# Kernel tuning notes

Measured on AMD Instinct MI355X. Metric: run time of the kernel, lower is better.

Reference implementation:

```python
import jax, jax.numpy as jnp
import numpy as np

B, T, C, H = 4, 2048, 1024, 16
HS = C // H  # head_size = 64
FF = 4 * C   # 4096
EPS = 1e-5


def _layernorm(x, g, b):
    mu = jnp.mean(x, axis=-1, keepdims=True)
    var = jnp.mean(jnp.square(x - mu), axis=-1, keepdims=True)
    return (x - mu) * jax.lax.rsqrt(var + EPS) * g + b


def setup_inputs() -> dict:
    key = jax.random.key(0)
    ks = jax.random.split(key, 12)
    s_in = 1.0 / np.sqrt(C)
    s_ff = 1.0 / np.sqrt(FF)
    return {
        "x": jax.random.normal(ks[0], (B, T, C), jnp.float32),
        # per-head projection weights stacked: [H, C, HS]
        "Wq": jax.random.normal(ks[1], (H, C, HS), jnp.float32) * s_in,
        "Wk": jax.random.normal(ks[2], (H, C, HS), jnp.float32) * s_in,
        "Wv": jax.random.normal(ks[3], (H, C, HS), jnp.float32) * s_in,
        "Wo": jax.random.normal(ks[4], (C, C), jnp.float32) * s_in,
        "bo": jnp.zeros((C,), jnp.float32),
        "g1": jnp.ones((C,), jnp.float32),
        "b1": jnp.zeros((C,), jnp.float32),
        "g2": jnp.ones((C,), jnp.float32),
        "b2": jnp.zeros((C,), jnp.float32),
        "W1": jax.random.normal(ks[5], (C, FF), jnp.float32) * s_in,
        "bf1": jnp.zeros((FF,), jnp.float32),
        "W2": jax.random.normal(ks[6], (FF, C), jnp.float32) * s_ff,
        "bf2": jnp.zeros((C,), jnp.float32),
    }


def reference(x, Wq, Wk, Wv, Wo, bo, g1, b1, g2, b2, W1, bf1, W2, bf2):
    # pre-norm
    h = _layernorm(x, g1, b1)                       # [B,T,C]
    q = jnp.einsum('btc,hcd->bhtd', h, Wq)          # [B,H,T,HS]
    k = jnp.einsum('btc,hcd->bhtd', h, Wk)
    v = jnp.einsum('btc,hcd->bhtd', h, Wv)
    w = jnp.einsum('bhtd,bhsd->bhts', q, k) * (HS ** -0.5)  # [B,H,T,S]
    mask = jnp.tril(jnp.ones((T, T), bool))          # causal tril
    w = jnp.where(mask[None, None], w, -jnp.inf)
    # NB: original code softmaxes over dim=1 of [B,T,T], i.e. the QUERY axis
    w = jax.nn.softmax(w, axis=-2)
    o = jnp.einsum('bhts,bhsd->bhtd', w, v)          # [B,H,T,HS]
    o = jnp.transpose(o, (0, 2, 1, 3)).reshape(B, T, C)  # concat heads
    x = x + o @ Wo + bo                              # residual 1 (dropout=0)
    f = _layernorm(x, g2, b2)
    ff = jax.nn.relu(f @ W1 + bf1) @ W2 + bf2        # FFN (dropout=0)
    return x + ff
```

## Files before the change

### kernel.cpp

```cpp
#include <hip/hip_runtime.h>


#define T_SEQ 2048
#define SCALE2 0.1803368801f

typedef __attribute__((ext_vector_type(8))) short short8;
typedef __attribute__((ext_vector_type(4))) float f32x4;

typedef __attribute__((address_space(1))) unsigned int g_u32;
typedef __attribute__((address_space(3))) unsigned int l_u32;

__device__ __forceinline__ unsigned short f2bf(float f) {
  union { float f; unsigned u; } x; x.f = f;
  unsigned r = (x.u + 0x7FFFu + ((x.u >> 16) & 1u)) >> 16;
  return (unsigned short)r;
}
__device__ __forceinline__ float bf2f(unsigned short u) {
  union { unsigned u; float f; } x; x.u = (unsigned)u << 16;
  return x.f;
}

__device__ __forceinline__ void g2lds16(const void* g, void* l) {
  __builtin_amdgcn_global_load_lds((g_u32*)g, (l_u32*)l, 16, 0, 0);
}

__device__ __forceinline__ int xcd_swz(int flat, int nwg) {
  if ((nwg & 7) != 0) return flat;
  return (flat & 7) * (nwg >> 3) + (flat >> 3);
}

template <int EPI>
__global__ __launch_bounds__(512, 2) void gemm256(
    const unsigned short* __restrict__ A, const unsigned short* __restrict__ Bt,
    int M, int N, int K,
    unsigned short* __restrict__ out16, const float* __restrict__ bias) {
  extern __shared__ unsigned short lds[];
  unsigned short* ldsA = lds;
  unsigned short* ldsB = lds + 2 * 16384;
  const int tid = threadIdx.x, lane = tid & 63, wid = tid >> 6;
  const int wm = wid >> 2, wn = wid & 3;
  const int nx = gridDim.x;
  const int flat = blockIdx.y * nx + blockIdx.x;
  const int swz = xcd_swz(flat, nx * gridDim.y);
  const int mBase = (swz / nx) * 256, nBase = (swz % nx) * 256;

  f32x4 acc[8][4];
#pragma unroll
  for (int i = 0; i < 8; ++i)
#pragma unroll
    for (int j = 0; j < 4; ++j)
#pragma unroll
      for (int e = 0; e < 4; ++e) acc[i][j][e] = 0.f;

  auto stage = [&](int buf, int kt) {
    const int k0 = kt << 6;
#pragma unroll
    for (int it = 0; it < 4; ++it) {
      int g = it * 512 + tid;
      int row = g >> 3, colL = g & 7;
      int col = colL ^ (row & 7);
      g2lds16(A + ((size_t)(mBase + row) * K + k0 + col * 8),
              &ldsA[buf * 16384 + (it * 512 + wid * 64) * 8]);
      g2lds16(Bt + ((size_t)(nBase + row) * K + k0 + col * 8),
              &ldsB[buf * 16384 + (it * 512 + wid * 64) * 8]);
    }
  };

  const int nKT = K >> 6;
  stage(0, 0);
  __syncthreads();
  int cur = 0;
  for (int kt = 0; kt < nKT; ++kt) {
    if (kt + 1 < nKT) stage(cur ^ 1, kt + 1);

    short8 bf[4][2];
#pragma unroll
    for (int fn = 0; fn < 4; ++fn)
#pragma unroll
      for (int ks = 0; ks < 2; ++ks) {
        int r = wn * 64 + fn * 16 + (lane & 15);
        int c = (ks * 4 + (lane >> 4)) ^ (r & 7);
        bf[fn][ks] = *(const short8*)&ldsB[cur * 16384 + r * 64 + c * 8];
      }
#pragma unroll
    for (int q = 0; q < 4; ++q) {
      short8 af[2][2];
#pragma unroll
      for (int mf = 0; mf < 2; ++mf)
#pragma unroll
        for (int ks = 0; ks < 2; ++ks) {
          int r = wm * 128 + q * 32 + mf * 16 + (lane & 15);
          int c = (ks * 4 + (lane >> 4)) ^ (r & 7);
          af[mf][ks] = *(const short8*)&ldsA[cur * 16384 + r * 64 + c * 8];
        }
      __builtin_amdgcn_s_setprio(1);
#pragma unroll
      for (int mf = 0; mf < 2; ++mf)
#pragma unroll
        for (int fn = 0; fn < 4; ++fn)
#pragma unroll
          for (int ks = 0; ks < 2; ++ks)
            acc[q * 2 + mf][fn] = __builtin_amdgcn_mfma_f32_16x16x32_bf16(
                af[mf][ks], bf[fn][ks], acc[q * 2 + mf][fn], 0, 0, 0);
      __builtin_amdgcn_s_setprio(0);
    }
    __syncthreads();
    cur ^= 1;
  }

#pragma unroll
  for (int am = 0; am < 8; ++am)
#pragma unroll
    for (int fn = 0; fn < 4; ++fn) {
      int col = nBase + wn * 64 + fn * 16 + (lane & 15);
      int row0 = mBase + wm * 128 + am * 16 + ((lane >> 4) << 2);
      if (EPI == 0) {
#pragma unroll
        for (int r = 0; r < 4; ++r)
          out16[(size_t)(row0 + r) * N + col] = f2bf(acc[am][fn][r]);
      } else {
        float bv = bias[col];
#pragma unroll
        for (int r = 0; r < 4; ++r)
          out16[(size_t)(row0 + r) * N + col] =
              f2bf(fmaxf(acc[am][fn][r] + bv, 0.f));
      }
    }
}

template <int EPI>
__global__ __launch_bounds__(256) void gemm_bt(
    const unsigned short* __restrict__ A, const unsigned short* __restrict__ Bt,
    int M, int N, int K,
    unsigned short* __restrict__ out16, float* __restrict__ outF,
    const float* __restrict__ bias, const float* __restrict__ resid) {
  __shared__ unsigned short ldsA[128 * 64];
  __shared__ unsigned short ldsB[128 * 64];
  const int tid = threadIdx.x;
  const int lane = tid & 63, wid = tid >> 6;
  const int wm = wid >> 1, wn = wid & 1;
  const int nx = gridDim.x;
  const int flat = blockIdx.y * nx + blockIdx.x;
  const int swz = xcd_swz(flat, nx * gridDim.y);
  const int mBase = (swz / nx) * 128, nBase = (swz % nx) * 128;

  f32x4 acc[4][4];
#pragma unroll
  for (int i = 0; i < 4; ++i)
#pragma unroll
    for (int j = 0; j < 4; ++j)
#pragma unroll
      for (int e = 0; e < 4; ++e) acc[i][j][e] = 0.f;

  const int nKT = K >> 6;
  for (int kt = 0; kt < nKT; ++kt) {
    const int k0 = kt << 6;
#pragma unroll
    for (int it = 0; it < 4; ++it) {
      int g = it * 256 + wid * 64 + lane;
      int row = g >> 3, colL = g & 7;
      int col = colL ^ (row & 7);
      g2lds16(A + ((size_t)(mBase + row) * K + k0 + col * 8),
              &ldsA[(it * 256 + wid * 64) * 8]);
      g2lds16(Bt + ((size_t)(nBase + row) * K + k0 + col * 8),
              &ldsB[(it * 256 + wid * 64) * 8]);
    }
    __syncthreads();

    short8 af[4][2], bf[4][2];
#pragma unroll
    for (int fm = 0; fm < 4; ++fm)
#pragma unroll
      for (int ks = 0; ks < 2; ++ks) {
        int r = wm * 64 + fm * 16 + (lane & 15);
        int c = (ks * 4 + (lane >> 4)) ^ (r & 7);
        af[fm][ks] = *(const short8*)&ldsA[r * 64 + c * 8];
      }
#pragma unroll
    for (int fn = 0; fn < 4; ++fn)
#pragma unroll
      for (int ks = 0; ks < 2; ++ks) {
        int r = wn * 64 + fn * 16 + (lane & 15);
        int c = (ks * 4 + (lane >> 4)) ^ (r & 7);
        bf[fn][ks] = *(const short8*)&ldsB[r * 64 + c * 8];
      }
    __builtin_amdgcn_s_setprio(1);
#pragma unroll
    for (int fm = 0; fm < 4; ++fm)
#pragma unroll
      for (int fn = 0; fn < 4; ++fn)
#pragma unroll
        for (int ks = 0; ks < 2; ++ks)
          acc[fm][fn] = __builtin_amdgcn_mfma_f32_16x16x32_bf16(
              af[fm][ks], bf[fn][ks], acc[fm][fn], 0, 0, 0);
    __builtin_amdgcn_s_setprio(0);
    __syncthreads();
  }

#pragma unroll
  for (int fm = 0; fm < 4; ++fm)
#pragma unroll
    for (int fn = 0; fn < 4; ++fn) {
      int col = nBase + wn * 64 + fn * 16 + (lane & 15);
      int row0 = mBase + wm * 64 + fm * 16 + ((lane >> 4) << 2);
      if (EPI == 0) {
#pragma unroll
        for (int r = 0; r < 4; ++r)
          out16[(size_t)(row0 + r) * N + col] = f2bf(acc[fm][fn][r]);
      } else if (EPI == 1) {
        float bv = bias[col];
#pragma unroll
        for (int r = 0; r < 4; ++r) {
          size_t idx = (size_t)(row0 + r) * N + col;
          outF[idx] = acc[fm][fn][r] + bv + resid[idx];
        }
      } else {
        float bv = bias[col];
#pragma unroll
        for (int r = 0; r < 4; ++r)
          out16[(size_t)(row0 + r) * N + col] =
              f2bf(fmaxf(acc[fm][fn][r] + bv, 0.f));
      }
    }
}

__global__ __launch_bounds__(256) void ln_bf16(
    const float* __restrict__ x, const float* __restrict__ gw,
    const float* __restrict__ bw, unsigned short* __restrict__ out) {
  __shared__ float red[8];
  const int row = blockIdx.x, tid = threadIdx.x;
  const float4 v = ((const float4*)(x + (size_t)row * 1024))[tid];
  float s = v.x + v.y + v.z + v.w;
  float q = v.x * v.x + v.y * v.y + v.z * v.z + v.w * v.w;
#pragma unroll
  for (int off = 32; off >= 1; off >>= 1) {
    s += __shfl_down(s, off);
    q += __shfl_down(q, off);
  }
  const int lane = tid & 63, wid = tid >> 6;
  if (lane == 0) { red[wid] = s; red[4 + wid] = q; }
  __syncthreads();
  float S = red[0] + red[1] + red[2] + red[3];
  float Q = red[4] + red[5] + red[6] + red[7];
  float mu = S * (1.f / 1024.f);
  float var = Q * (1.f / 1024.f) - mu * mu;
  float rs = rsqrtf(var + 1e-5f);
  int c = tid * 4;
  ushort4 ov;
  ov.x = f2bf((v.x - mu) * rs * gw[c + 0] + bw[c + 0]);
  ov.y = f2bf((v.y - mu) * rs * gw[c + 1] + bw[c + 1]);
  ov.z = f2bf((v.z - mu) * rs * gw[c + 2] + bw[c + 2]);
  ov.w = f2bf((v.w - mu) * rs * gw[c + 3] + bw[c + 3]);
  *(ushort4*)&out[(size_t)row * 1024 + c] = ov;
}

__global__ __launch_bounds__(256) void pack_qkv(
    const float* __restrict__ Wq, const float* __restrict__ Wk,
    const float* __restrict__ Wv, unsigned short* __restrict__ out) {
  __shared__ float tile[64 * 65];
  const int tid = threadIdx.x;
  const float* W = (blockIdx.z == 0) ? Wq : (blockIdx.z == 1) ? Wk : Wv;
  const int h = blockIdx.y, r0 = blockIdx.x * 64;
#pragma unroll
  for (int it = 0; it < 4; ++it) {
    int e4 = it * 256 + tid;
    int r = e4 >> 4, c4 = e4 & 15;
    float4 v = *(const float4*)&W[((size_t)h * 1024 + r0 + r) * 64 + c4 * 4];
    tile[r * 65 + c4 * 4 + 0] = v.x;
    tile[r * 65 + c4 * 4 + 1] = v.y;
    tile[r * 65 + c4 * 4 + 2] = v.z;
    tile[r * 65 + c4 * 4 + 3] = v.w;
  }
  __syncthreads();
#pragma unroll
  for (int it = 0; it < 4; ++it) {
    int e4 = it * 256 + tid;
    int d = e4 >> 4, r4 = e4 & 15;
    ushort4 ov;
    ov.x = f2bf(tile[(r4 * 4 + 0) * 65 + d]);
    ov.y = f2bf(tile[(r4 * 4 + 1) * 65 + d]);
    ov.z = f2bf(tile[(r4 * 4 + 2) * 65 + d]);
    ov.w = f2bf(tile[(r4 * 4 + 3) * 65 + d]);
    *(ushort4*)&out[(size_t)(blockIdx.z * 1024 + h * 64 + d) * 1024 + r0 +
                    r4 * 4] = ov;
  }
}

__global__ __launch_bounds__(256) void transpose_cast(
    const float* __restrict__ in, unsigned short* __restrict__ out, int R,
    int C) {
  __shared__ float tile[64 * 65];
  const int tid = threadIdx.x;
  const int r0 = blockIdx.x * 64, c0 = blockIdx.y * 64;
#pragma unroll
  for (int it = 0; it < 4; ++it) {
    int e4 = it * 256 + tid;
    int r = e4 >> 4, c4 = e4 & 15;
    float4 v = *(const float4*)&in[(size_t)(r0 + r) * C + c0 + c4 * 4];
    tile[r * 65 + c4 * 4 + 0] = v.x;
    tile[r * 65 + c4 * 4 + 1] = v.y;
    tile[r * 65 + c4 * 4 + 2] = v.z;
    tile[r * 65 + c4 * 4 + 3] = v.w;
  }
  __syncthreads();
#pragma unroll
  for (int it = 0; it < 4; ++it) {
    int e4 = it * 256 + tid;
    int c = e4 >> 4, r4 = e4 & 15;
    ushort4 ov;
    ov.x = f2bf(tile[(r4 * 4 + 0) * 65 + c]);
    ov.y = f2bf(tile[(r4 * 4 + 1) * 65 + c]);
    ov.z = f2bf(tile[(r4 * 4 + 2) * 65 + c]);
    ov.w = f2bf(tile[(r4 * 4 + 3) * 65 + c]);
    *(ushort4*)&out[(size_t)(c0 + c) * R + r0 + r4 * 4] = ov;
  }
}

__global__ __launch_bounds__(256) void vtrans(
    const unsigned short* __restrict__ qkv, const float* __restrict__ linv,
    unsigned short* __restrict__ vT) {
  __shared__ unsigned short tile[64 * 66];
  const int tid = threadIdx.x;
  const int bh = blockIdx.y, b = bh >> 4, h = bh & 15;
  const int t0 = blockIdx.x * 64;
#pragma unroll
  for (int it = 0; it < 8; ++it) {
    int e2 = it * 256 + tid;
    int r = e2 >> 5, c2 = e2 & 31;
    unsigned v = *(const unsigned*)&qkv[(size_t)(b * T_SEQ + t0 + r) * 3072 +
                                        2048 + h * 64 + c2 * 2];
    float li = linv[(size_t)bh * T_SEQ + t0 + r];
    unsigned short lo = f2bf(bf2f((unsigned short)(v & 0xffff)) * li);
    unsigned short hi = f2bf(bf2f((unsigned short)(v >> 16)) * li);
    *(unsigned*)&tile[r * 66 + c2 * 2] = (unsigned)lo | ((unsigned)hi << 16);
  }
  __syncthreads();
#pragma unroll
  for (int it = 0; it < 8; ++it) {
    int e2 = it * 256 + tid;
    int d = e2 >> 5, t2 = e2 & 31;
    unsigned short a = tile[(t2 * 2) * 66 + d];
    unsigned short bb = tile[(t2 * 2 + 1) * 66 + d];
    unsigned pk = (unsigned)a | ((unsigned)bb << 16);
    *(unsigned*)&vT[(size_t)(bh * 64 + d) * T_SEQ + t0 + t2 * 2] = pk;
  }
}

__global__ __launch_bounds__(256) void attn_stats(
    const unsigned short* __restrict__ qkv, float* __restrict__ linvOut) {
  __shared__ unsigned short qt[4][2][64 * 64];
  __shared__ float redL[4][2][64];
  const int tid = threadIdx.x, lane = tid & 63, w = tid >> 6;
  const int bh = blockIdx.y, b = bh >> 4, h = bh & 15;
  const int sx = blockIdx.x;
  const int sA = sx * 64, sB = (31 - sx) * 64;
  const int nT = 32 - sx;
  const int bDiag = 31 - 2 * sx;

  short8 kfA[4][2], kfB[4][2];
#pragma unroll
  for (int fn = 0; fn < 4; ++fn)
#pragma unroll
    for (int ks = 0; ks < 2; ++ks) {
      int d = 1024 + h * 64 + ks * 32 + ((lane >> 4) << 3);
      kfA[fn][ks] = *(const short8*)&qkv[(size_t)(b * T_SEQ + sA + fn * 16 +
                                                  (lane & 15)) * 3072 + d];
      kfB[fn][ks] = *(const short8*)&qkv[(size_t)(b * T_SEQ + sB + fn * 16 +
                                                  (lane & 15)) * 3072 + d];
    }
  float lA[4] = {0.f, 0.f, 0.f, 0.f}, lB[4] = {0.f, 0.f, 0.f, 0.f};

  auto stageQ = [&](int buf, int idx) {
    int t0 = sA + idx * 64;
#pragma unroll
    for (int it = 0; it < 8; ++it) {
      int g = it * 64 + lane;
      int row = g >> 3;
      int col = (g & 7) ^ (row & 7);
      g2lds16(qkv + ((size_t)(b * T_SEQ + t0 + row) * 3072 + h * 64 + col * 8),
              &qt[w][buf][it * 512]);
    }
  };

  auto accum = [&](const short8 (&af)[2], const short8 (&kf)[4][2],
                   float (&lacc)[4], int sBase, int t0, int mf, bool diag) {
    f32x4 sc[4];
#pragma unroll
    for (int fn = 0; fn < 4; ++fn)
#pragma unroll
      for (int e = 0; e < 4; ++e) sc[fn][e] = 0.f;
    __builtin_amdgcn_s_setprio(1);
#pragma unroll
    for (int fn = 0; fn < 4; ++fn)
#pragma unroll
      for (int ks = 0; ks < 2; ++ks)
        sc[fn] = __builtin_amdgcn_mfma_f32_16x16x32_bf16(af[ks], kf[fn][ks],
                                                         sc[fn], 0, 0, 0);
    __builtin_amdgcn_s_setprio(0);
    const int tRow = t0 + mf * 16 + ((lane >> 4) << 2);
    if (diag) {
#pragma unroll
      for (int fn = 0; fn < 4; ++fn) {
        int s = sBase + fn * 16 + (lane & 15);
#pragma unroll
        for (int r = 0; r < 4; ++r) {
          float e = exp2f(sc[fn][r] * SCALE2);
          lacc[fn] += (tRow + r >= s) ? e : 0.f;
        }
      }
    } else {
#pragma unroll
      for (int fn = 0; fn < 4; ++fn)
#pragma unroll
        for (int r = 0; r < 4; ++r) lacc[fn] += exp2f(sc[fn][r] * SCALE2);
    }
  };

  int idx = w, cur = 0;
  stageQ(0, idx);
  for (; idx < nT; idx += 4, cur ^= 1) {
    if (idx + 4 < nT) {
      stageQ(cur ^ 1, idx + 4);
      asm volatile("s_waitcnt vmcnt(8)" ::: "memory");
    } else {
      asm volatile("s_waitcnt vmcnt(0)" ::: "memory");
    }
    const int t0 = sA + idx * 64;
    const bool doB = idx >= bDiag;
#pragma unroll
    for (int mf = 0; mf < 4; ++mf) {
      short8 af[2];
#pragma unroll
      for (int ks = 0; ks < 2; ++ks) {
        int r = mf * 16 + (lane & 15);
        int c = (ks * 4 + (lane >> 4)) ^ (r & 7);
        af[ks] = *(const short8*)&qt[w][cur][r * 64 + c * 8];
      }
      accum(af, kfA, lA, sA, t0, mf, idx == 0);
      if (doB) accum(af, kfB, lB, sB, t0, mf, idx == bDiag);
    }
  }
#pragma unroll
  for (int fn = 0; fn < 4; ++fn) {
    lA[fn] += __shfl_down(lA[fn], 32);
    lA[fn] += __shfl_down(lA[fn], 16);
    lB[fn] += __shfl_down(lB[fn], 32);
    lB[fn] += __shfl_down(lB[fn], 16);
  }
  if (lane < 16) {
#pragma unroll
    for (int fn = 0; fn < 4; ++fn) {
      redL[w][0][fn * 16 + lane] = lA[fn];
      redL[w][1][fn * 16 + lane] = lB[fn];
    }
  }
  __syncthreads();
  if (tid < 128) {
    int which = tid >> 6;
    float l = redL[0][which][lane] + redL[1][which][lane] +
              redL[2][which][lane] + redL[3][which][lane];
    int sbase = (which == 0) ? sA : sB;
    linvOut[(size_t)bh * T_SEQ + sbase + lane] = 1.f / l;
  }
}

__global__ __launch_bounds__(256, 2) void attn_pv(
    const unsigned short* __restrict__ qkv, const unsigned short* __restrict__ vT,
    unsigned short* __restrict__ o) {
  __shared__ unsigned short kbuf[2][64 * 64];
  __shared__ unsigned short vbuf[2][64 * 64];
  __shared__ unsigned short pl[256 * 64];
  const int tid = threadIdx.x, lane = tid & 63, wid = tid >> 6;
  const int bh = blockIdx.y, b = bh >> 4, h = bh & 15;
  const int bx = blockIdx.x;
  const int tA = bx * 128, tB = (15 - bx) * 128;
  const int nSTA = 2 * bx + 2, nSTB = 32 - 2 * bx;

  short8 qfA[2][2], qfB[2][2];
#pragma unroll
  for (int mf = 0; mf < 2; ++mf)
#pragma unroll
    for (int ks = 0; ks < 2; ++ks) {
      int d = h * 64 + ks * 32 + ((lane >> 4) << 3);
      int rloc = wid * 32 + mf * 16 + (lane & 15);
      qfA[mf][ks] =
          *(const short8*)&qkv[(size_t)(b * T_SEQ + tA + rloc) * 3072 + d];
      qfB[mf][ks] =
          *(const short8*)&qkv[(size_t)(b * T_SEQ + tB + rloc) * 3072 + d];
    }
  f32x4 oaccA[2][4], oaccB[2][4];
#pragma unroll
  for (int i = 0; i < 2; ++i)
#pragma unroll
    for (int j = 0; j < 4; ++j)
#pragma unroll
      for (int e = 0; e < 4; ++e) { oaccA[i][j][e] = 0.f; oaccB[i][j][e] = 0.f; }

  auto stage = [&](int buf, int st) {
#pragma unroll
    for (int it = 0; it < 2; ++it) {
      int g = it * 256 + tid;
      int row = g >> 3, colL = g & 7;
      int col = colL ^ (row & 7);
      g2lds16(qkv + ((size_t)(b * T_SEQ + st * 64 + row) * 3072 + 1024 +
                     h * 64 + col * 8),
              &kbuf[buf][(it * 256 + wid * 64) * 8]);
      g2lds16(vT + ((size_t)(bh * 64 + row) * T_SEQ + st * 64 + col * 8),
              &vbuf[buf][(it * 256 + wid * 64) * 8]);
    }
  };

  auto qkstore = [&](const short8 (&qf)[2][2], int rowBase, int tBase, int s0,
                     bool maskNeeded, int cur) {
    f32x4 sc[2][4];
#pragma unroll
    for (int i = 0; i < 2; ++i)
#pragma unroll
      for (int j = 0; j < 4; ++j)
#pragma unroll
        for (int e = 0; e < 4; ++e) sc[i][j][e] = 0.f;
    __builtin_amdgcn_s_setprio(1);
#pragma unroll
    for (int fn = 0; fn < 4; ++fn)
#pragma unroll
      for (int ks = 0; ks < 2; ++ks) {
        int r = fn * 16 + (lane & 15);
        int c = (ks * 4 + (lane >> 4)) ^ (r & 7);
        short8 kfr = *(const short8*)&kbuf[cur][r * 64 + c * 8];
        sc[0][fn] = __builtin_amdgcn_mfma_f32_16x16x32_bf16(qf[0][ks], kfr,
                                                            sc[0][fn], 0, 0, 0);
        sc[1][fn] = __builtin_amdgcn_mfma_f32_16x16x32_bf16(qf[1][ks], kfr,
                                                            sc[1][fn], 0, 0, 0);
      }
    __builtin_amdgcn_s_setprio(0);
#pragma unroll
    for (int fn = 0; fn < 4; ++fn) {
      int sg = s0 + fn * 16 + (lane & 15);
      int colb = (fn * 16 + (lane & 15)) * 2;
#pragma unroll
      for (int mf = 0; mf < 2; ++mf) {
        int rowB = rowBase + wid * 32 + mf * 16 + ((lane >> 4) << 2);
        int tRow = tBase + wid * 32 + mf * 16 + ((lane >> 4) << 2);
#pragma unroll
        for (int r = 0; r < 4; ++r) {
          float p = exp2f(sc[mf][fn][r] * SCALE2);
          if (maskNeeded) p = (tRow + r >= sg) ? p : 0.f;
          int row = rowB + r;
          int byteoff = row * 128 + (colb ^ ((row & 7) << 4));
          *(unsigned short*)((char*)pl + byteoff) = f2bf(p);
        }
      }
    }
  };

  stage(0, 0);
  int cur = 0;
  __syncthreads();

  for (int st = 0; st < nSTB; ++st) {
    const int s0 = st * 64;
    const bool doA = st < nSTA;

    if (doA) qkstore(qfA, 0, tA, s0, st >= nSTA - 2, cur);
    qkstore(qfB, 128, tB, s0, st >= nSTB - 2, cur);
    __syncthreads();

    if (st + 1 < nSTB) stage(cur ^ 1, st + 1);

    __builtin_amdgcn_s_setprio(1);
#pragma unroll
    for (int ks = 0; ks < 2; ++ks) {
      short8 paA[2], paB[2];
#pragma unroll
      for (int mf = 0; mf < 2; ++mf) {
        int rowa = wid * 32 + mf * 16 + (lane & 15);
        int kb = ks * 64 + ((lane >> 4) << 4);
        paB[mf] = *(const short8*)((const char*)pl + (128 + rowa) * 128 +
                                   (kb ^ ((rowa & 7) << 4)));
        if (doA)
          paA[mf] = *(const short8*)((const char*)pl + rowa * 128 +
                                     (kb ^ ((rowa & 7) << 4)));
      }
#pragma unroll
      for (int df = 0; df < 4; ++df) {
        int r = df * 16 + (lane & 15);
        int c = (ks * 4 + (lane >> 4)) ^ (r & 7);
        short8 vb = *(const short8*)&vbuf[cur][r * 64 + c * 8];
        oaccB[0][df] = __builtin_amdgcn_mfma_f32_16x16x32_bf16(paB[0], vb,
                                                               oaccB[0][df], 0, 0, 0);
        oaccB[1][df] = __builtin_amdgcn_mfma_f32_16x16x32_bf16(paB[1], vb,
                                                               oaccB[1][df], 0, 0, 0);
        if (doA) {
          oaccA[0][df] = __builtin_amdgcn_mfma_f32_16x16x32_bf16(paA[0], vb,
                                                                 oaccA[0][df], 0, 0, 0);
          oaccA[1][df] = __builtin_amdgcn_mfma_f32_16x16x32_bf16(paA[1], vb,
                                                                 oaccA[1][df], 0, 0, 0);
        }
      }
    }
    __builtin_amdgcn_s_setprio(0);
    __syncthreads();
    cur ^= 1;
  }
#pragma unroll
  for (int mf = 0; mf < 2; ++mf)
#pragma unroll
    for (int df = 0; df < 4; ++df) {
      int d = h * 64 + df * 16 + (lane & 15);
      int ra = tA + wid * 32 + mf * 16 + ((lane >> 4) << 2);
      int rb = tB + wid * 32 + mf * 16 + ((lane >> 4) << 2);
#pragma unroll
      for (int r = 0; r < 4; ++r) {
        o[(size_t)(b * T_SEQ + ra + r) * 1024 + d] = f2bf(oaccA[mf][df][r]);
        o[(size_t)(b * T_SEQ + rb + r) * 1024 + d] = f2bf(oaccB[mf][df][r]);
      }
    }
}

extern "C" void kernel_launch(void* const* d_in, const int* in_sizes, int n_in,
                              void* d_out, int out_size, void* d_ws,
                              size_t ws_size, hipStream_t stream) {
  const float* x = (const float*)d_in[0];
  const float* Wq = (const float*)d_in[1];
  const float* Wk = (const float*)d_in[2];
  const float* Wv = (const float*)d_in[3];
  const float* Wo = (const float*)d_in[4];
  const float* bo = (const float*)d_in[5];
  const float* g1 = (const float*)d_in[6];
  const float* b1 = (const float*)d_in[7];
  const float* g2 = (const float*)d_in[8];
  const float* b2 = (const float*)d_in[9];
  const float* W1 = (const float*)d_in[10];
  const float* bf1 = (const float*)d_in[11];
  const float* W2 = (const float*)d_in[12];
  const float* bf2 = (const float*)d_in[13];
  float* out = (float*)d_out;

  char* ws = (char*)d_ws;
  size_t off = 0;
  auto alloc = [&](size_t bytes) {
    char* p = ws + off;
    off += (bytes + 255) & ~(size_t)255;
    return p;
  };
  unsigned short* Wqkv = (unsigned short*)alloc(3072ull * 1024 * 2);
  unsigned short* WoT = (unsigned short*)alloc(1024ull * 1024 * 2);
  unsigned short* W1T = (unsigned short*)alloc(4096ull * 1024 * 2);
  unsigned short* W2T = (unsigned short*)alloc(1024ull * 4096 * 2);
  unsigned short* hbuf = (unsigned short*)alloc(8192ull * 1024 * 2);
  char* regionE = alloc(8192ull * 3072 * 2 + 64ull * 64 * 2048 * 2);
  unsigned short* qkv = (unsigned short*)regionE;
  unsigned short* vT = (unsigned short*)(regionE + 8192ull * 3072 * 2);
  unsigned short* act = (unsigned short*)regionE;
  float* lbuf = (float*)alloc(64ull * 2048 * 4);
  float* x1 = (float*)alloc(8192ull * 1024 * 4);
  unsigned short* fbuf = (unsigned short*)alloc(8192ull * 1024 * 2);
  unsigned short* obuf = hbuf;

  (void)in_sizes; (void)n_in; (void)out_size; (void)ws_size;

  pack_qkv<<<dim3(16, 16, 3), 256, 0, stream>>>(Wq, Wk, Wv, Wqkv);
  transpose_cast<<<dim3(16, 16), 256, 0, stream>>>(Wo, WoT, 1024, 1024);
  transpose_cast<<<dim3(16, 64), 256, 0, stream>>>(W1, W1T, 1024, 4096);
  transpose_cast<<<dim3(64, 16), 256, 0, stream>>>(W2, W2T, 4096, 1024);
  ln_bf16<<<8192, 256, 0, stream>>>(x, g1, b1, hbuf);
  gemm256<0><<<dim3(12, 32), 512, 131072, stream>>>(hbuf, Wqkv, 8192, 3072,
                                                    1024, qkv, nullptr);
  attn_stats<<<dim3(16, 64), 256, 0, stream>>>(qkv, lbuf);
  vtrans<<<dim3(32, 64), 256, 0, stream>>>(qkv, lbuf, vT);
  attn_pv<<<dim3(8, 64), 256, 0, stream>>>(qkv, vT, obuf);
  gemm_bt<1><<<dim3(8, 64), 256, 0, stream>>>(obuf, WoT, 8192, 1024, 1024,
                                              nullptr, x1, bo, x);
  ln_bf16<<<8192, 256, 0, stream>>>(x1, g2, b2, fbuf);
  gemm256<2><<<dim3(16, 32), 512, 131072, stream>>>(fbuf, W1T, 8192, 4096,
                                                    1024, act, bf1);
  gemm_bt<1><<<dim3(8, 64), 256, 0, stream>>>(act, W2T, 8192, 1024, 4096,
                                              nullptr, out, bf2, x1);
}
```

Before: 435.8 us.

## Generalize gemm256 over N-tile width, drop gemm_bt, restructure attention stats schedule

Templates the 256-row GEMM on its N-tile width and adds a residual epilogue, so the QKV, output-projection and FFN-down GEMMs all use the double-buffered 512-thread kernel (256x128 tiles) instead of the single-buffered 128x128 gemm_bt. attn_stats is restructured so all four waves share one double-buffered Q tile stream in LDS, each wave owns distinct key rows, and the cross-wave reduction is removed. Both attention kernels gain XCD-aware block swizzling. The risk is lower occupancy or tail imbalance with 256-row tiles on the smaller GEMMs, and load imbalance across blocks in the new stats schedule.

```diff
diff --git a/kernel.cpp b/kernel.cpp
--- a/kernel.cpp
+++ b/kernel.cpp
@@ -29,11 +29,14 @@
   return (flat & 7) * (nwg >> 3) + (flat >> 3);
 }
 
-template <int EPI>
+template <int EPI, int BN>
 __global__ __launch_bounds__(512, 2) void gemm256(
     const unsigned short* __restrict__ A, const unsigned short* __restrict__ Bt,
     int M, int N, int K,
-    unsigned short* __restrict__ out16, const float* __restrict__ bias) {
+    unsigned short* __restrict__ out16, float* __restrict__ outF,
+    const float* __restrict__ bias, const float* __restrict__ resid) {
+  constexpr int WN = BN / 4;
+  constexpr int FN = WN / 16;
   extern __shared__ unsigned short lds[];
   unsigned short* ldsA = lds;
   unsigned short* ldsB = lds + 2 * 16384;
@@ -42,13 +45,13 @@
   const int nx = gridDim.x;
   const int flat = blockIdx.y * nx + blockIdx.x;
   const int swz = xcd_swz(flat, nx * gridDim.y);
-  const int mBase = (swz / nx) * 256, nBase = (swz % nx) * 256;
-
-  f32x4 acc[8][4];
+  const int mBase = (swz / nx) * 256, nBase = (swz % nx) * BN;
+
+  f32x4 acc[8][FN];
 #pragma unroll
   for (int i = 0; i < 8; ++i)
 #pragma unroll
-    for (int j = 0; j < 4; ++j)
+    for (int j = 0; j < FN; ++j)
 #pragma unroll
       for (int e = 0; e < 4; ++e) acc[i][j][e] = 0.f;
 
@@ -61,8 +64,14 @@
       int col = colL ^ (row & 7);
       g2lds16(A + ((size_t)(mBase + row) * K + k0 + col * 8),
               &ldsA[buf * 16384 + (it * 512 + wid * 64) * 8]);
+    }
+#pragma unroll
+    for (int it = 0; it < (BN * 8) / 512; ++it) {
+      int g = it * 512 + tid;
+      int row = g >> 3, colL = g & 7;
+      int col = colL ^ (row & 7);
       g2lds16(Bt + ((size_t)(nBase + row) * K + k0 + col * 8),
-              &ldsB[buf * 16384 + (it * 512 + wid * 64) * 8]);
+              &ldsB[buf * (BN * 64) + (it * 512 + wid * 64) * 8]);
     }
   };
 
@@ -73,14 +82,14 @@
   for (int kt = 0; kt < nKT; ++kt) {
     if (kt + 1 < nKT) stage(cur ^ 1, kt + 1);
 
-    short8 bf[4][2];
-#pragma unroll
-    for (int fn = 0; fn < 4; ++fn)
+    short8 bf[FN][2];
+#pragma unroll
+    for (int fn = 0; fn < FN; ++fn)
 #pragma unroll
       for (int ks = 0; ks < 2; ++ks) {
-        int r = wn * 64 + fn * 16 + (lane & 15);
+        int r = wn * WN + fn * 16 + (lane & 15);
         int c = (ks * 4 + (lane >> 4)) ^ (r & 7);
-        bf[fn][ks] = *(const short8*)&ldsB[cur * 16384 + r * 64 + c * 8];
+        bf[fn][ks] = *(const short8*)&ldsB[cur * (BN * 64) + r * 64 + c * 8];
       }
 #pragma unroll
     for (int q = 0; q < 4; ++q) {
@@ -97,7 +106,7 @@
 #pragma unroll
       for (int mf = 0; mf < 2; ++mf)
 #pragma unroll
-        for (int fn = 0; fn < 4; ++fn)
+        for (int fn = 0; fn < FN; ++fn)
 #pragma unroll
           for (int ks = 0; ks < 2; ++ks)
             acc[q * 2 + mf][fn] = __builtin_amdgcn_mfma_f32_16x16x32_bf16(
@@ -111,115 +120,26 @@
 #pragma unroll
   for (int am = 0; am < 8; ++am)
 #pragma unroll
-    for (int fn = 0; fn < 4; ++fn) {
-      int col = nBase + wn * 64 + fn * 16 + (lane & 15);
+    for (int fn = 0; fn < FN; ++fn) {
+      int col = nBase + wn * WN + fn * 16 + (lane & 15);
       int row0 = mBase + wm * 128 + am * 16 + ((lane >> 4) << 2);
       if (EPI == 0) {
 #pragma unroll
         for (int r = 0; r < 4; ++r)
           out16[(size_t)(row0 + r) * N + col] = f2bf(acc[am][fn][r]);
+      } else if (EPI == 1) {
+        float bv = bias[col];
+#pragma unroll
+        for (int r = 0; r < 4; ++r) {
+          size_t idx = (size_t)(row0 + r) * N + col;
+          outF[idx] = acc[am][fn][r] + bv + resid[idx];
+        }
       } else {
         float bv = bias[col];
 #pragma unroll
         for (int r = 0; r < 4; ++r)
           out16[(size_t)(row0 + r) * N + col] =
               f2bf(fmaxf(acc[am][fn][r] + bv, 0.f));
-      }
-    }
-}
-
-template <int EPI>
-__global__ __launch_bounds__(256) void gemm_bt(
-    const unsigned short* __restrict__ A, const unsigned short* __restrict__ Bt,
-    int M, int N, int K,
-    unsigned short* __restrict__ out16, float* __restrict__ outF,
-    const float* __restrict__ bias, const float* __restrict__ resid) {
-  __shared__ unsigned short ldsA[128 * 64];
-  __shared__ unsigned short ldsB[128 * 64];
-  const int tid = threadIdx.x;
-  const int lane = tid & 63, wid = tid >> 6;
-  const int wm = wid >> 1, wn = wid & 1;
-  const int nx = gridDim.x;
-  const int flat = blockIdx.y * nx + blockIdx.x;
-  const int swz = xcd_swz(flat, nx * gridDim.y);
-  const int mBase = (swz / nx) * 128, nBase = (swz % nx) * 128;
-
-  f32x4 acc[4][4];
-#pragma unroll
-  for (int i = 0; i < 4; ++i)
-#pragma unroll
-    for (int j = 0; j < 4; ++j)
-#pragma unroll
-      for (int e = 0; e < 4; ++e) acc[i][j][e] = 0.f;
-
-  const int nKT = K >> 6;
-  for (int kt = 0; kt < nKT; ++kt) {
-    const int k0 = kt << 6;
-#pragma unroll
-    for (int it = 0; it < 4; ++it) {
-      int g = it * 256 + wid * 64 + lane;
-      int row = g >> 3, colL = g & 7;
-      int col = colL ^ (row & 7);
-      g2lds16(A + ((size_t)(mBase + row) * K + k0 + col * 8),
-              &ldsA[(it * 256 + wid * 64) * 8]);
-      g2lds16(Bt + ((size_t)(nBase + row) * K + k0 + col * 8),
-              &ldsB[(it * 256 + wid * 64) * 8]);
-    }
-    __syncthreads();
-
-    short8 af[4][2], bf[4][2];
-#pragma unroll
-    for (int fm = 0; fm < 4; ++fm)
-#pragma unroll
-      for (int ks = 0; ks < 2; ++ks) {
-        int r = wm * 64 + fm * 16 + (lane & 15);
-        int c = (ks * 4 + (lane >> 4)) ^ (r & 7);
-        af[fm][ks] = *(const short8*)&ldsA[r * 64 + c * 8];
-      }
-#pragma unroll
-    for (int fn = 0; fn < 4; ++fn)
-#pragma unroll
-      for (int ks = 0; ks < 2; ++ks) {
-        int r = wn * 64 + fn * 16 + (lane & 15);
-        int c = (ks * 4 + (lane >> 4)) ^ (r & 7);
-        bf[fn][ks] = *(const short8*)&ldsB[r * 64 + c * 8];
-      }
-    __builtin_amdgcn_s_setprio(1);
-#pragma unroll
-    for (int fm = 0; fm < 4; ++fm)
-#pragma unroll
-      for (int fn = 0; fn < 4; ++fn)
-#pragma unroll
-        for (int ks = 0; ks < 2; ++ks)
-          acc[fm][fn] = __builtin_amdgcn_mfma_f32_16x16x32_bf16(
-              af[fm][ks], bf[fn][ks], acc[fm][fn], 0, 0, 0);
-    __builtin_amdgcn_s_setprio(0);
-    __syncthreads();
-  }
-
-#pragma unroll
-  for (int fm = 0; fm < 4; ++fm)
-#pragma unroll
-    for (int fn = 0; fn < 4; ++fn) {
-      int col = nBase + wn * 64 + fn * 16 + (lane & 15);
-      int row0 = mBase + wm * 64 + fm * 16 + ((lane >> 4) << 2);
-      if (EPI == 0) {
-#pragma unroll
-        for (int r = 0; r < 4; ++r)
-          out16[(size_t)(row0 + r) * N + col] = f2bf(acc[fm][fn][r]);
-      } else if (EPI == 1) {
-        float bv = bias[col];
-#pragma unroll
-        for (int r = 0; r < 4; ++r) {
-          size_t idx = (size_t)(row0 + r) * N + col;
-          outF[idx] = acc[fm][fn][r] + bv + resid[idx];
-        }
-      } else {
-        float bv = bias[col];
-#pragma unroll
-        for (int r = 0; r < 4; ++r)
-          out16[(size_t)(row0 + r) * N + col] =
-              f2bf(fmaxf(acc[fm][fn][r] + bv, 0.f));
       }
     }
 }
@@ -348,14 +268,14 @@
 
 __global__ __launch_bounds__(256) void attn_stats(
     const unsigned short* __restrict__ qkv, float* __restrict__ linvOut) {
-  __shared__ unsigned short qt[4][2][64 * 64];
-  __shared__ float redL[4][2][64];
+  __shared__ unsigned short qt[2][64 * 64];
   const int tid = threadIdx.x, lane = tid & 63, w = tid >> 6;
-  const int bh = blockIdx.y, b = bh >> 4, h = bh & 15;
-  const int sx = blockIdx.x;
-  const int sA = sx * 64, sB = (31 - sx) * 64;
-  const int nT = 32 - sx;
-  const int bDiag = 31 - 2 * sx;
+  const int f = xcd_swz(blockIdx.y * 8 + blockIdx.x, 512);
+  const int q = f & 7, bh = f >> 3;
+  const int b = bh >> 4, h = bh & 15;
+  const int sxA = q * 4 + w, sxB = 31 - sxA;
+  const int sA = sxA * 64, sB = sxB * 64;
+  const int it0 = (q <= 3) ? 4 * q : 28 - 4 * q;
 
   short8 kfA[4][2], kfB[4][2];
 #pragma unroll
@@ -370,15 +290,15 @@
     }
   float lA[4] = {0.f, 0.f, 0.f, 0.f}, lB[4] = {0.f, 0.f, 0.f, 0.f};
 
-  auto stageQ = [&](int buf, int idx) {
-    int t0 = sA + idx * 64;
-#pragma unroll
-    for (int it = 0; it < 8; ++it) {
-      int g = it * 64 + lane;
+  auto stageQ = [&](int buf, int ti) {
+    int t0 = ti * 64;
+#pragma unroll
+    for (int it = 0; it < 2; ++it) {
+      int g = it * 256 + tid;
       int row = g >> 3;
       int col = (g & 7) ^ (row & 7);
       g2lds16(qkv + ((size_t)(b * T_SEQ + t0 + row) * 3072 + h * 64 + col * 8),
-              &qt[w][buf][it * 512]);
+              &qt[buf][(it * 256 + w * 64) * 8]);
     }
   };
 
@@ -416,29 +336,29 @@
     }
   };
 
-  int idx = w, cur = 0;
-  stageQ(0, idx);
-  for (; idx < nT; idx += 4, cur ^= 1) {
-    if (idx + 4 < nT) {
-      stageQ(cur ^ 1, idx + 4);
-      asm volatile("s_waitcnt vmcnt(8)" ::: "memory");
-    } else {
-      asm volatile("s_waitcnt vmcnt(0)" ::: "memory");
-    }
-    const int t0 = sA + idx * 64;
-    const bool doB = idx >= bDiag;
-#pragma unroll
-    for (int mf = 0; mf < 4; ++mf) {
-      short8 af[2];
-#pragma unroll
-      for (int ks = 0; ks < 2; ++ks) {
-        int r = mf * 16 + (lane & 15);
-        int c = (ks * 4 + (lane >> 4)) ^ (r & 7);
-        af[ks] = *(const short8*)&qt[w][cur][r * 64 + c * 8];
-      }
-      accum(af, kfA, lA, sA, t0, mf, idx == 0);
-      if (doB) accum(af, kfB, lB, sB, t0, mf, idx == bDiag);
-    }
+  stageQ(0, it0);
+  __syncthreads();
+  int cur = 0;
+  for (int ti = it0; ti < 32; ++ti) {
+    if (ti + 1 < 32) stageQ(cur ^ 1, ti + 1);
+    const bool doA = ti >= sxA, doB = ti >= sxB;
+    if (doA | doB) {
+      const int t0g = ti * 64;
+#pragma unroll
+      for (int mf = 0; mf < 4; ++mf) {
+        short8 af[2];
+#pragma unroll
+        for (int ks = 0; ks < 2; ++ks) {
+          int r = mf * 16 + (lane & 15);
+          int c = (ks * 4 + (lane >> 4)) ^ (r & 7);
+          af[ks] = *(const short8*)&qt[cur][r * 64 + c * 8];
+        }
+        if (doA) accum(af, kfA, lA, sA, t0g, mf, ti == sxA);
+        if (doB) accum(af, kfB, lB, sB, t0g, mf, ti == sxB);
+      }
+    }
+    __syncthreads();
+    cur ^= 1;
   }
 #pragma unroll
   for (int fn = 0; fn < 4; ++fn) {
@@ -450,17 +370,9 @@
   if (lane < 16) {
 #pragma unroll
     for (int fn = 0; fn < 4; ++fn) {
-      redL[w][0][fn * 16 + lane] = lA[fn];
-      redL[w][1][fn * 16 + lane] = lB[fn];
-    }
-  }
-  __syncthreads();
-  if (tid < 128) {
-    int which = tid >> 6;
-    float l = redL[0][which][lane] + redL[1][which][lane] +
-              redL[2][which][lane] + redL[3][which][lane];
-    int sbase = (which == 0) ? sA : sB;
-    linvOut[(size_t)bh * T_SEQ + sbase + lane] = 1.f / l;
+      linvOut[(size_t)bh * T_SEQ + sA + fn * 16 + lane] = 1.f / lA[fn];
+      linvOut[(size_t)bh * T_SEQ + sB + fn * 16 + lane] = 1.f / lB[fn];
+    }
   }
 }
 
@@ -471,8 +383,9 @@
   __shared__ unsigned short vbuf[2][64 * 64];
   __shared__ unsigned short pl[256 * 64];
   const int tid = threadIdx.x, lane = tid & 63, wid = tid >> 6;
-  const int bh = blockIdx.y, b = bh >> 4, h = bh & 15;
-  const int bx = blockIdx.x;
+  const int f = xcd_swz(blockIdx.y * 8 + blockIdx.x, 512);
+  const int bx = f & 7, bh = f >> 3;
+  const int b = bh >> 4, h = bh & 15;
   const int tA = bx * 128, tB = (15 - bx) * 128;
   const int nSTA = 2 * bx + 2, nSTB = 32 - 2 * bx;
 
@@ -659,21 +572,24 @@
 
   (void)in_sizes; (void)n_in; (void)out_size; (void)ws_size;
 
+  const size_t LDS128 = (2 * 16384 + 2 * 128 * 64) * 2;
+  const size_t LDS256 = (2 * 16384 + 2 * 256 * 64) * 2;
+
   pack_qkv<<<dim3(16, 16, 3), 256, 0, stream>>>(Wq, Wk, Wv, Wqkv);
   transpose_cast<<<dim3(16, 16), 256, 0, stream>>>(Wo, WoT, 1024, 1024);
   transpose_cast<<<dim3(16, 64), 256, 0, stream>>>(W1, W1T, 1024, 4096);
   transpose_cast<<<dim3(64, 16), 256, 0, stream>>>(W2, W2T, 4096, 1024);
   ln_bf16<<<8192, 256, 0, stream>>>(x, g1, b1, hbuf);
-  gemm256<0><<<dim3(12, 32), 512, 131072, stream>>>(hbuf, Wqkv, 8192, 3072,
-                                                    1024, qkv, nullptr);
-  attn_stats<<<dim3(16, 64), 256, 0, stream>>>(qkv, lbuf);
+  gemm256<0, 128><<<dim3(24, 32), 512, LDS128, stream>>>(
+      hbuf, Wqkv, 8192, 3072, 1024, qkv, nullptr, nullptr, nullptr);
+  attn_stats<<<dim3(8, 64), 256, 0, stream>>>(qkv, lbuf);
   vtrans<<<dim3(32, 64), 256, 0, stream>>>(qkv, lbuf, vT);
   attn_pv<<<dim3(8, 64), 256, 0, stream>>>(qkv, vT, obuf);
-  gemm_bt<1><<<dim3(8, 64), 256, 0, stream>>>(obuf, WoT, 8192, 1024, 1024,
-                                              nullptr, x1, bo, x);
+  gemm256<1, 128><<<dim3(8, 32), 512, LDS128, stream>>>(
+      obuf, WoT, 8192, 1024, 1024, nullptr, x1, bo, x);
   ln_bf16<<<8192, 256, 0, stream>>>(x1, g2, b2, fbuf);
-  gemm256<2><<<dim3(16, 32), 512, 131072, stream>>>(fbuf, W1T, 8192, 4096,
-                                                    1024, act, bf1);
-  gemm_bt<1><<<dim3(8, 64), 256, 0, stream>>>(act, W2T, 8192, 1024, 4096,
-                                              nullptr, out, bf2, x1);
-}
+  gemm256<2, 256><<<dim3(16, 32), 512, LDS256, stream>>>(
+      fbuf, W1T, 8192, 4096, 1024, act, nullptr, bf1, nullptr);
+  gemm256<1, 128><<<dim3(8, 32), 512, LDS128, stream>>>(
+      act, W2T, 8192, 1024, 4096, nullptr, out, bf2, x1);
+}
```

Result: slower. 477.5 us (+9.6%).
